# Performance work log

Hardware: AMD Instinct MI355X
Metric: run time of the kernel (lower is better)

The kernel has to match this reference:

```python
import jax, jax.numpy as jnp
import numpy as np

B, T, C = 2, 2048, 1024
N_HEAD = 16
HEAD_DIM = C // N_HEAD


def setup_inputs() -> dict:
    key = jax.random.key(0)
    k1, k2, k3 = jax.random.split(key, 3)
    x = jax.random.normal(k1, (B, T, C), dtype=jnp.float32)
    w_attn = jax.random.normal(k2, (C, 3 * C), dtype=jnp.float32) * 0.02
    b_attn = jnp.zeros((3 * C,), dtype=jnp.float32)
    w_proj = jax.random.normal(k3, (C, C), dtype=jnp.float32) * 0.02
    b_proj = jnp.zeros((C,), dtype=jnp.float32)
    return {"x": x, "w_attn": w_attn, "b_attn": b_attn, "w_proj": w_proj, "b_proj": b_proj}


def reference(x, w_attn, b_attn, w_proj, b_proj):
    Bz, Tz, Cz = x.shape
    qkv = x @ w_attn + b_attn                       # [B, T, 3C]
    q, k, v = jnp.split(qkv, 3, axis=-1)
    # [B, H, T, D]
    q = q.reshape(Bz, Tz, N_HEAD, HEAD_DIM).transpose(0, 2, 1, 3)
    k = k.reshape(Bz, Tz, N_HEAD, HEAD_DIM).transpose(0, 2, 1, 3)
    v = v.reshape(Bz, Tz, N_HEAD, HEAD_DIM).transpose(0, 2, 1, 3)
    scale = 1.0 / np.sqrt(HEAD_DIM).astype(np.float32)
    att = jnp.einsum('bhqd,bhkd->bhqk', q, k) * scale  # [B, H, T, T]
    causal = jnp.tril(jnp.ones((Tz, Tz), dtype=bool))
    att = jnp.where(causal[None, None], att, -jnp.inf)
    att = jax.nn.softmax(att, axis=-1)
    y = jnp.einsum('bhqk,bhkd->bhqd', att, v)          # [B, H, T, D]
    y = y.transpose(0, 2, 1, 3).reshape(Bz, Tz, Cz)
    return y @ w_proj + b_proj
```

## Files before the change

kernel.cpp:

```cpp
#include <hip/hip_runtime.h>
#include <stdint.h>

#define T_SEQ 2048
#define NH 16
#define HD 64
#define M_DIM 4096
#define K_DIM 1024

typedef __attribute__((ext_vector_type(8))) short bf16x8;
typedef __attribute__((ext_vector_type(4))) float f32x4;
typedef __attribute__((ext_vector_type(4))) unsigned short u16x4;

__device__ __forceinline__ unsigned short f2bf(float f) {
  union { float f; uint32_t u; } x; x.f = f;
  uint32_t u = x.u;
  return (unsigned short)((u + 0x7fffu + ((u >> 16) & 1u)) >> 16);
}

#define GLOAD16(g, l) __builtin_amdgcn_global_load_lds( \
    (const __attribute__((address_space(1))) unsigned int*)(g), \
    (__attribute__((address_space(3))) unsigned int*)(l), 16, 0, 0)

__global__ __launch_bounds__(256) void convert_x_kernel(const float* __restrict__ src,
                                                        unsigned short* __restrict__ dst) {
  int idx = (blockIdx.x * 256 + threadIdx.x) * 4;
  f32x4 v = *(const f32x4*)(src + idx);
  u16x4 o;
  #pragma unroll
  for (int i = 0; i < 4; ++i) o[i] = f2bf(v[i]);
  *(u16x4*)(dst + idx) = o;
}

__global__ __launch_bounds__(256) void transpose_w_kernel(const float* __restrict__ src,
                                                          unsigned short* __restrict__ dst,
                                                          int R, int Cn) {
  __shared__ float tile[64][65];
  const int r0 = blockIdx.y * 64, c0 = blockIdx.x * 64;
  const int t = threadIdx.x;
  const int rr = t >> 4;
  const int c4 = (t & 15) * 4;
  #pragma unroll
  for (int p = 0; p < 4; ++p) {
    f32x4 v = *(const f32x4*)(src + (size_t)(r0 + p * 16 + rr) * Cn + c0 + c4);
    #pragma unroll
    for (int i = 0; i < 4; ++i) tile[p * 16 + rr][c4 + i] = v[i];
  }
  __syncthreads();
  #pragma unroll
  for (int p = 0; p < 4; ++p) {
    const int cl = p * 16 + rr;
    u16x4 o;
    #pragma unroll
    for (int i = 0; i < 4; ++i) o[i] = f2bf(tile[c4 + i][cl]);
    *(u16x4*)(dst + (size_t)(c0 + cl) * R + r0 + c4) = o;
  }
}

template <int MODE>
__global__ __launch_bounds__(256) void gemm_bt_kernel(
    const unsigned short* __restrict__ A,
    const unsigned short* __restrict__ Bt,
    const float* __restrict__ bias,
    unsigned short* __restrict__ qout,
    unsigned short* __restrict__ kout,
    unsigned short* __restrict__ vTout,
    float* __restrict__ fout) {
  __shared__ __align__(16) unsigned short As[128 * 32];
  __shared__ __align__(16) unsigned short Bs[128 * 32];
  const int t = threadIdx.x;
  const int w = t >> 6, l = t & 63;
  const int wr = w >> 1, wc = w & 1;
  const int lr = l & 15, lg = l >> 4;
  const int br = blockIdx.y, bc = blockIdx.x;

  f32x4 acc[4][4];
  const f32x4 zf = {0.f, 0.f, 0.f, 0.f};
  #pragma unroll
  for (int i = 0; i < 4; ++i)
    #pragma unroll
    for (int j = 0; j < 4; ++j) acc[i][j] = zf;

  const int ce = (t & 3) * 8;
  const unsigned short* Abase = A + (size_t)(br * 128) * K_DIM;
  const unsigned short* Bbase = Bt + (size_t)(bc * 128) * K_DIM;

  for (int k0 = 0; k0 < K_DIM; k0 += 32) {
    #pragma unroll
    for (int it = 0; it < 2; ++it) {
      const int u = it * 256 + t;
      const int row = u >> 2;
      GLOAD16(Abase + (size_t)row * K_DIM + k0 + ce, As + u * 8);
      GLOAD16(Bbase + (size_t)row * K_DIM + k0 + ce, Bs + u * 8);
    }
    __syncthreads();
    bf16x8 af[4], bfv[4];
    #pragma unroll
    for (int f = 0; f < 4; ++f) {
      af[f]  = *(const bf16x8*)(As + (wr * 64 + f * 16 + lr) * 32 + lg * 8);
      bfv[f] = *(const bf16x8*)(Bs + (wc * 64 + f * 16 + lr) * 32 + lg * 8);
    }
    #pragma unroll
    for (int fr = 0; fr < 4; ++fr)
      #pragma unroll
      for (int fc = 0; fc < 4; ++fc)
        acc[fr][fc] = __builtin_amdgcn_mfma_f32_16x16x32_bf16(af[fr], bfv[fc], acc[fr][fc], 0, 0, 0);
    __syncthreads();
  }

  #pragma unroll
  for (int fr = 0; fr < 4; ++fr) {
    #pragma unroll
    for (int fc = 0; fc < 4; ++fc) {
      const int m0 = br * 128 + wr * 64 + fr * 16 + lg * 4;
      const int n  = bc * 128 + wc * 64 + fc * 16 + lr;
      if (MODE == 0) {
        const int which = n >> 10, rem = n & 1023;
        const int h = rem >> 6, d = rem & 63;
        const int b = m0 >> 11, tt0 = m0 & 2047;
        const int bh = b * NH + h;
        if (which == 2) {
          u16x4 pack;
          #pragma unroll
          for (int r = 0; r < 4; ++r) pack[r] = f2bf(acc[fr][fc][r] + bias[n]);
          *(u16x4*)(vTout + ((size_t)bh * HD + d) * T_SEQ + tt0) = pack;
        } else {
          unsigned short* o = (which == 0) ? qout : kout;
          #pragma unroll
          for (int r = 0; r < 4; ++r)
            o[((size_t)bh * T_SEQ + tt0 + r) * HD + d] = f2bf(acc[fr][fc][r] + bias[n]);
        }
      } else {
        #pragma unroll
        for (int r = 0; r < 4; ++r)
          fout[(size_t)(m0 + r) * 1024 + n] = acc[fr][fc][r] + bias[n];
      }
    }
  }
}

__global__ __launch_bounds__(256) void flash_attn_kernel(
    const unsigned short* __restrict__ qg,
    const unsigned short* __restrict__ kg,
    const unsigned short* __restrict__ vTg,
    unsigned short* __restrict__ yg) {
  __shared__ __align__(16) unsigned short Ks[2][64 * 64];
  __shared__ __align__(16) unsigned short Vs[2][64 * 64];
  __shared__ __align__(16) unsigned short P[4][16][64];

  const int t = threadIdx.x;
  const int w = t >> 6, l = t & 63;
  const int lr = l & 15, lg = l >> 4;
  const int lb = (blockIdx.x & 7) * 64 + (blockIdx.x >> 3);
  const int pid = lb & 15;
  const int bh = lb >> 4;
  const int swz = lr & 7;

  const int srow0 = t >> 3;
  const int sch = t & 7;

  const size_t kgb = (size_t)bh * T_SEQ * HD;
  const size_t vgb = (size_t)bh * HD * T_SEQ;

  #pragma unroll 1
  for (int ph = 0; ph < 2; ++ph) {
    const int qt = ph ? (31 - pid) : pid;
    const int nt = qt + 1;
    const int qw = qt * 64 + w * 16;
    const int qrow = qw + lr;

    const size_t qoff = ((size_t)bh * T_SEQ + qw + lr) * HD + lg * 8;
    const bf16x8 qf0 = *(const bf16x8*)(qg + qoff);
    const bf16x8 qf1 = *(const bf16x8*)(qg + qoff + 32);

    f32x4 acc[4];
    const f32x4 zf = {0.f, 0.f, 0.f, 0.f};
    #pragma unroll
    for (int i = 0; i < 4; ++i) acc[i] = zf;
    float m_run = -3e38f, l_run = 0.f;

    #pragma unroll
    for (int sh = 0; sh < 2; ++sh) {
      const int row = sh * 32 + srow0;
      const int sc = (sch ^ (row & 7)) * 8;
      GLOAD16(kg + kgb + (size_t)row * HD + sc, Ks[0] + row * 64 + sch * 8);
      GLOAD16(vTg + vgb + (size_t)row * T_SEQ + sc, Vs[0] + row * 64 + sch * 8);
    }
    __syncthreads();

    int cur = 0;
    #pragma unroll 1
    for (int it = 0; it < nt; ++it) {
      const int kv0 = it * 64;
      if (it + 1 < nt) {
        const int kvn = kv0 + 64;
        #pragma unroll
        for (int sh = 0; sh < 2; ++sh) {
          const int row = sh * 32 + srow0;
          const int sc = (sch ^ (row & 7)) * 8;
          GLOAD16(kg + kgb + (size_t)(kvn + row) * HD + sc, Ks[cur ^ 1] + row * 64 + sch * 8);
          GLOAD16(vTg + vgb + (size_t)row * T_SEQ + kvn + sc, Vs[cur ^ 1] + row * 64 + sch * 8);
        }
      }

      f32x4 s[4];
      __builtin_amdgcn_s_setprio(1);
      #pragma unroll
      for (int fc = 0; fc < 4; ++fc) {
        const unsigned short* kr = Ks[cur] + (fc * 16 + lr) * 64;
        const bf16x8 k0v = *(const bf16x8*)(kr + ((lg ^ swz) * 8));
        const bf16x8 k1v = *(const bf16x8*)(kr + (((lg + 4) ^ swz) * 8));
        f32x4 sv = zf;
        sv = __builtin_amdgcn_mfma_f32_16x16x32_bf16(k0v, qf0, sv, 0, 0, 0);
        sv = __builtin_amdgcn_mfma_f32_16x16x32_bf16(k1v, qf1, sv, 0, 0, 0);
        s[fc] = sv;
      }
      __builtin_amdgcn_s_setprio(0);

      float pvv[4][4];
      float mt = -3e38f;
      #pragma unroll
      for (int fc = 0; fc < 4; ++fc)
        #pragma unroll
        for (int r = 0; r < 4; ++r) {
          float sv = s[fc][r] * 0.125f;
          const int tkv = kv0 + fc * 16 + lg * 4 + r;
          sv = (tkv > qrow) ? -3e38f : sv;
          pvv[fc][r] = sv;
          mt = fmaxf(mt, sv);
        }
      mt = fmaxf(mt, __shfl_xor(mt, 16));
      mt = fmaxf(mt, __shfl_xor(mt, 32));
      const float m_new = fmaxf(m_run, mt);
      float ssum = 0.f;
      #pragma unroll
      for (int fc = 0; fc < 4; ++fc) {
        u16x4 pk;
        #pragma unroll
        for (int r = 0; r < 4; ++r) {
          const float e = __expf(pvv[fc][r] - m_new);
          ssum += e;
          pk[r] = f2bf(e);
        }
        *(u16x4*)&P[w][lr][(fc * 16 + lg * 4) ^ ((lr & 3) << 4)] = pk;
      }
      ssum += __shfl_xor(ssum, 16);
      ssum += __shfl_xor(ssum, 32);
      const float fac = __expf(m_run - m_new);
      l_run = l_run * fac + ssum;
      m_run = m_new;
      float frs[4];
      #pragma unroll
      for (int r = 0; r < 4; ++r) frs[r] = __shfl(fac, lg * 4 + r);
      #pragma unroll
      for (int fd = 0; fd < 4; ++fd)
        #pragma unroll
        for (int r = 0; r < 4; ++r) acc[fd][r] *= frs[r];

      const bf16x8 pa0 = *(const bf16x8*)&P[w][lr][(lg * 8) ^ ((lr & 3) << 4)];
      const bf16x8 pa1 = *(const bf16x8*)&P[w][lr][(32 + lg * 8) ^ ((lr & 3) << 4)];
      __builtin_amdgcn_s_setprio(1);
      #pragma unroll
      for (int fd = 0; fd < 4; ++fd) {
        const unsigned short* vr = Vs[cur] + (fd * 16 + lr) * 64;
        const bf16x8 v0 = *(const bf16x8*)(vr + ((lg ^ swz) * 8));
        const bf16x8 v1 = *(const bf16x8*)(vr + (((lg + 4) ^ swz) * 8));
        acc[fd] = __builtin_amdgcn_mfma_f32_16x16x32_bf16(pa0, v0, acc[fd], 0, 0, 0);
        acc[fd] = __builtin_amdgcn_mfma_f32_16x16x32_bf16(pa1, v1, acc[fd], 0, 0, 0);
      }
      __builtin_amdgcn_s_setprio(0);
      __syncthreads();
      cur ^= 1;
    }

    const int b = bh >> 4, h = bh & 15;
    #pragma unroll
    for (int r = 0; r < 4; ++r) {
      const float lv = __shfl(l_run, lg * 4 + r);
      const float linv = 1.f / lv;
      const int tt = qw + lg * 4 + r;
      #pragma unroll
      for (int fd = 0; fd < 4; ++fd) {
        const int d = fd * 16 + lr;
        yg[(((size_t)b * T_SEQ + tt) * NH + h) * HD + d] = f2bf(acc[fd][r] * linv);
      }
    }
    __syncthreads();
  }
}

extern "C" void kernel_launch(void* const* d_in, const int* in_sizes, int n_in,
                              void* d_out, int out_size, void* d_ws, size_t ws_size,
                              hipStream_t stream) {
  (void)in_sizes; (void)n_in; (void)out_size; (void)ws_size;
  const float* x      = (const float*)d_in[0];
  const float* w_attn = (const float*)d_in[1];
  const float* b_attn = (const float*)d_in[2];
  const float* w_proj = (const float*)d_in[3];
  const float* b_proj = (const float*)d_in[4];
  float* out = (float*)d_out;

  char* ws = (char*)d_ws;
  unsigned short* xb     = (unsigned short*)(ws);
  unsigned short* wqkvT  = (unsigned short*)(ws + (8ull  << 20));
  unsigned short* wprojT = (unsigned short*)(ws + (14ull << 20));
  unsigned short* qb     = (unsigned short*)(ws + (16ull << 20));
  unsigned short* kb     = (unsigned short*)(ws + (24ull << 20));
  unsigned short* vT     = (unsigned short*)(ws + (32ull << 20));
  unsigned short* yb     = (unsigned short*)(ws + (40ull << 20));

  convert_x_kernel<<<4096, 256, 0, stream>>>(x, xb);
  transpose_w_kernel<<<dim3(48, 16), 256, 0, stream>>>(w_attn, wqkvT, 1024, 3072);
  transpose_w_kernel<<<dim3(16, 16), 256, 0, stream>>>(w_proj, wprojT, 1024, 1024);
  gemm_bt_kernel<0><<<dim3(24, 32), 256, 0, stream>>>(xb, wqkvT, b_attn, qb, kb, vT, nullptr);
  flash_attn_kernel<<<512, 256, 0, stream>>>(qb, kb, vT, yb);
  gemm_bt_kernel<1><<<dim3(8, 32), 256, 0, stream>>>(yb, wprojT, b_proj, nullptr, nullptr, nullptr, out);
}
```

Before: 216.2 us.

## Streamline attention softmax with lazy rescaling, exp2, prescaled Q, packed bf16 cvt

Folds the softmax scale and log2(e) into Q in the QKV GEMM epilogue so the attention loop can use raw exp2 with no per-element multiply. Causal masking is applied only on the diagonal tile. Max/rescale work runs only when some lane's max grows by more than a threshold (lazy rescaling), and the row-sum reduction is deferred to the end. P is packed to bf16 with the hardware v_cvt_pk_bf16_f32 instruction, which is meant to cut VALU work in the softmax. In exchange, exponents can reach up to 2^8 before a rescale, which carries a small precision and overflow risk.

```diff
diff --git a/kernel.cpp b/kernel.cpp
--- a/kernel.cpp
+++ b/kernel.cpp
@@ -15,6 +15,12 @@
   union { float f; uint32_t u; } x; x.f = f;
   uint32_t u = x.u;
   return (unsigned short)((u + 0x7fffu + ((u >> 16) & 1u)) >> 16);
+}
+
+__device__ __forceinline__ uint32_t cvtpk_bf16(float a, float b) {
+  uint32_t r;
+  asm("v_cvt_pk_bf16_f32 %0, %1, %2" : "=v"(r) : "v"(a), "v"(b));
+  return r;
 }
 
 #define GLOAD16(g, l) __builtin_amdgcn_global_load_lds( \
@@ -125,9 +131,10 @@
           *(u16x4*)(vTout + ((size_t)bh * HD + d) * T_SEQ + tt0) = pack;
         } else {
           unsigned short* o = (which == 0) ? qout : kout;
+          const float sc = (which == 0) ? 0.18033688011112042f : 1.0f;
           #pragma unroll
           for (int r = 0; r < 4; ++r)
-            o[((size_t)bh * T_SEQ + tt0 + r) * HD + d] = f2bf(acc[fr][fc][r] + bias[n]);
+            o[((size_t)bh * T_SEQ + tt0 + r) * HD + d] = f2bf((acc[fr][fc][r] + bias[n]) * sc);
         }
       } else {
         #pragma unroll
@@ -160,6 +167,7 @@
 
   const size_t kgb = (size_t)bh * T_SEQ * HD;
   const size_t vgb = (size_t)bh * HD * T_SEQ;
+  const f32x4 zf = {0.f, 0.f, 0.f, 0.f};
 
   #pragma unroll 1
   for (int ph = 0; ph < 2; ++ph) {
@@ -173,10 +181,10 @@
     const bf16x8 qf1 = *(const bf16x8*)(qg + qoff + 32);
 
     f32x4 acc[4];
-    const f32x4 zf = {0.f, 0.f, 0.f, 0.f};
     #pragma unroll
     for (int i = 0; i < 4; ++i) acc[i] = zf;
-    float m_run = -3e38f, l_run = 0.f;
+    float m_run = 0.f;
+    float l_part = 0.f;
 
     #pragma unroll
     for (int sh = 0; sh < 2; ++sh) {
@@ -216,45 +224,49 @@
       }
       __builtin_amdgcn_s_setprio(0);
 
-      float pvv[4][4];
-      float mt = -3e38f;
+      if (it == nt - 1) {
+        #pragma unroll
+        for (int fc = 0; fc < 4; ++fc)
+          #pragma unroll
+          for (int r = 0; r < 4; ++r) {
+            const int tkv = kv0 + fc * 16 + lg * 4 + r;
+            if (tkv > qrow) s[fc][r] = -1e30f;
+          }
+      }
+
+      float mt = s[0][0];
       #pragma unroll
       for (int fc = 0; fc < 4; ++fc)
         #pragma unroll
-        for (int r = 0; r < 4; ++r) {
-          float sv = s[fc][r] * 0.125f;
-          const int tkv = kv0 + fc * 16 + lg * 4 + r;
-          sv = (tkv > qrow) ? -3e38f : sv;
-          pvv[fc][r] = sv;
-          mt = fmaxf(mt, sv);
-        }
-      mt = fmaxf(mt, __shfl_xor(mt, 16));
-      mt = fmaxf(mt, __shfl_xor(mt, 32));
-      const float m_new = fmaxf(m_run, mt);
-      float ssum = 0.f;
+        for (int r = 0; r < 4; ++r) mt = fmaxf(mt, s[fc][r]);
+      if (__any(mt > m_run + 8.f)) {
+        float mrow = fmaxf(mt, __shfl_xor(mt, 16));
+        mrow = fmaxf(mrow, __shfl_xor(mrow, 32));
+        const float m_new = fmaxf(m_run, mrow);
+        const float fac = __builtin_amdgcn_exp2f(m_run - m_new);
+        l_part *= fac;
+        float frs[4];
+        #pragma unroll
+        for (int r = 0; r < 4; ++r) frs[r] = __shfl(fac, lg * 4 + r);
+        #pragma unroll
+        for (int fd = 0; fd < 4; ++fd)
+          #pragma unroll
+          for (int r = 0; r < 4; ++r) acc[fd][r] *= frs[r];
+        m_run = m_new;
+      }
+
       #pragma unroll
       for (int fc = 0; fc < 4; ++fc) {
-        u16x4 pk;
-        #pragma unroll
-        for (int r = 0; r < 4; ++r) {
-          const float e = __expf(pvv[fc][r] - m_new);
-          ssum += e;
-          pk[r] = f2bf(e);
-        }
-        *(u16x4*)&P[w][lr][(fc * 16 + lg * 4) ^ ((lr & 3) << 4)] = pk;
-      }
-      ssum += __shfl_xor(ssum, 16);
-      ssum += __shfl_xor(ssum, 32);
-      const float fac = __expf(m_run - m_new);
-      l_run = l_run * fac + ssum;
-      m_run = m_new;
-      float frs[4];
-      #pragma unroll
-      for (int r = 0; r < 4; ++r) frs[r] = __shfl(fac, lg * 4 + r);
-      #pragma unroll
-      for (int fd = 0; fd < 4; ++fd)
-        #pragma unroll
-        for (int r = 0; r < 4; ++r) acc[fd][r] *= frs[r];
+        float e0 = __builtin_amdgcn_exp2f(s[fc][0] - m_run);
+        float e1 = __builtin_amdgcn_exp2f(s[fc][1] - m_run);
+        float e2 = __builtin_amdgcn_exp2f(s[fc][2] - m_run);
+        float e3 = __builtin_amdgcn_exp2f(s[fc][3] - m_run);
+        l_part += (e0 + e1) + (e2 + e3);
+        uint2 pk;
+        pk.x = cvtpk_bf16(e0, e1);
+        pk.y = cvtpk_bf16(e2, e3);
+        *(uint2*)&P[w][lr][(fc * 16 + lg * 4) ^ ((lr & 3) << 4)] = pk;
+      }
 
       const bf16x8 pa0 = *(const bf16x8*)&P[w][lr][(lg * 8) ^ ((lr & 3) << 4)];
       const bf16x8 pa1 = *(const bf16x8*)&P[w][lr][(32 + lg * 8) ^ ((lr & 3) << 4)];
@@ -272,10 +284,14 @@
       cur ^= 1;
     }
 
+    float lsum = l_part;
+    lsum += __shfl_xor(lsum, 16);
+    lsum += __shfl_xor(lsum, 32);
+
     const int b = bh >> 4, h = bh & 15;
     #pragma unroll
     for (int r = 0; r < 4; ++r) {
-      const float lv = __shfl(l_run, lg * 4 + r);
+      const float lv = __shfl(lsum, lg * 4 + r);
       const float linv = 1.f / lv;
       const int tt = qw + lg * 4 + r;
       #pragma unroll
```

Measured after the change: 202.2 us. -6.5%, faster.
